# Performance work log

Measured on AMD Instinct MI355X. Metric: run time of the kernel, lower is better.

Reference implementation:

```python
import jax, jax.numpy as jnp
import numpy as np

B, T, IN, H, L, OUT, PRED, FN = 512, 96, 64, 512, 2, 1, 24, 32


def setup_inputs() -> dict:
    key = jax.random.key(0)
    ks = jax.random.split(key, 12)
    sc = 0.02
    n = lambda i, shape: jax.random.normal(ks[i], shape, jnp.float32) * sc
    return {
        "x": jax.random.normal(ks[0], (B, T, IN), jnp.float32),
        "station_id": jax.random.randint(ks[1], (B,), 0, 26, jnp.int32),
        "W_hidden": n(2, (H, IN)), "b_hidden": jnp.zeros((H,), jnp.float32),
        "embed": n(3, (26, H)),
        "W_ih": n(4, (L, 4 * H, H)), "W_hh": n(5, (L, 4 * H, H)),
        "b_ih": jnp.zeros((L, 4 * H), jnp.float32), "b_hh": jnp.zeros((L, 4 * H), jnp.float32),
        "conv_W": n(6, (FN, T - 1)), "conv_b": jnp.zeros((FN,), jnp.float32),
        "W1": n(7, (FN, H)), "b1": jnp.zeros((FN,), jnp.float32),
        "W2": n(8, (H, H + FN)), "b2": jnp.zeros((H,), jnp.float32),
        "W_out": n(9, (T * OUT, H)), "b_out": jnp.zeros((T * OUT,), jnp.float32),
    }


def _lstm(xc, W_ih, W_hh, b_ih, b_hh):
    # xc: [B, T, H]; multi-layer LSTM, PyTorch gate order i,f,g,o
    n_layers = W_ih.shape[0]
    h0 = jnp.zeros((n_layers, xc.shape[0], W_hh.shape[-1]), xc.dtype)

    def step(carry, xt):
        h, c = carry  # [L, B, H]
        inp = xt
        hs, cs = [], []
        for l in range(n_layers):
            g = inp @ W_ih[l].T + h[l] @ W_hh[l].T + b_ih[l] + b_hh[l]
            i, f, gg, o = jnp.split(g, 4, axis=-1)
            cn = jax.nn.sigmoid(f) * c[l] + jax.nn.sigmoid(i) * jnp.tanh(gg)
            hn = jax.nn.sigmoid(o) * jnp.tanh(cn)
            hs.append(hn); cs.append(cn)
            inp = hn
        return (jnp.stack(hs), jnp.stack(cs)), inp  # emit last-layer h

    _, outs = jax.lax.scan(step, (h0, h0), jnp.swapaxes(xc, 0, 1))
    return jnp.swapaxes(outs, 0, 1)  # [B, T, H] last-layer hidden states


def reference(x, station_id, W_hidden, b_hidden, embed, W_ih, W_hh, b_ih, b_hh,
              conv_W, conv_b, W1, b1, W2, b2, W_out, b_out):
    b, t, _ = x.shape
    hdim = W_hidden.shape[0]
    fn = conv_W.shape[0]
    xc = jax.nn.relu(x @ W_hidden.T + b_hidden)
    xc = xc + embed[station_id][:, None, :]
    hs_seq = _lstm(xc, W_ih, W_hh, b_ih, b_hh)          # [B, T, H]
    Hmat = jax.nn.relu(hs_seq[:, :-1, :])                # [B, T-1, H]
    htt = hs_seq[:, -1, :]                               # [B, H]
    # Conv2d(1, FN, (T-1, 1)) over [B,1,T-1,H] == contraction over time
    conv = jax.nn.relu(jnp.einsum('bth,ft->bfh', Hmat, conv_W) + conv_b[None, :, None])
    # original does .view(-1, feat_size, filter_num): raw reshape, not transpose
    feat = conv.reshape(b, hdim, fn)                     # [B, H, FN]
    w = (htt @ W1.T + b1)[:, None, :]                    # [B, 1, FN]
    alpha = jax.nn.sigmoid(jnp.sum(feat * w, axis=2))    # [B, H]
    v = jnp.sum(alpha[:, :, None] * feat, axis=1)        # [B, FN]
    new_ht = jnp.concatenate([htt, v], axis=1) @ W2.T + b2
    ypred = (new_ht @ W_out.T + b_out)[:, -PRED * OUT:]
    return ypred
```

## Files before the change

kernel.cpp:

```cpp
#include <hip/hip_runtime.h>
#include <math.h>

namespace {

constexpr int B = 512, T = 96, IN = 64, H = 512, G4 = 2048;
constexpr int FN = 32, KC = 544, NPRED = 24, TM1 = T - 1;
constexpr int BH = B * H;

typedef __attribute__((ext_vector_type(8))) short s8v;
typedef __attribute__((ext_vector_type(16))) float f16v;

__device__ __forceinline__ float sigf(float x) { return 1.0f / (1.0f + __expf(-x)); }
__device__ __forceinline__ float tanhfast(float x) {
  x = fminf(fmaxf(x, -15.f), 15.f);
  float e = __expf(2.0f * x);
  return (e - 1.0f) / (e + 1.0f);
}
__device__ __forceinline__ unsigned short bf16_rne(float f) {
  unsigned u = __float_as_uint(f);
  u += 0x7fffu + ((u >> 16) & 1u);
  return (unsigned short)(u >> 16);
}
__device__ __forceinline__ void split8(const float4& x, const float4& y, s8v& hi, s8v& lo) {
  float vs[8] = {x.x, x.y, x.z, x.w, y.x, y.y, y.z, y.w};
#pragma unroll
  for (int j = 0; j < 8; ++j) {
    unsigned ub = __float_as_uint(vs[j]);
    hi[j] = (short)(ub >> 16);
    lo[j] = (short)bf16_rne(vs[j] - __uint_as_float(ub & 0xffff0000u));
  }
}

__global__ __launch_bounds__(256) void k_xc(
    const float* __restrict__ x, const int* __restrict__ sid,
    const float* __restrict__ Wh, const float* __restrict__ bh,
    const float* __restrict__ emb, float* __restrict__ planes) {
  constexpr int RWS = 64;
  int gid = blockIdx.x;
  int half = gid & 1;
  int row0 = (gid >> 1) * RWS;
  int tid = threadIdx.x;
  int h = half * 256 + tid;
  __shared__ float sx[RWS][IN];
  {
    const float4* xsrc = (const float4*)(x + (size_t)row0 * IN);
    float4* sdst = (float4*)(&sx[0][0]);
    for (int i = tid; i < RWS * IN / 4; i += 256) sdst[i] = xsrc[i];
  }
  float4 w[16];
  const float* wr = Wh + (size_t)h * IN;
#pragma unroll
  for (int j = 0; j < 16; ++j) w[j] = *(const float4*)(wr + j * 4);
  float b0 = bh[h];
  const float* ep = emb + h;
  __syncthreads();
#pragma unroll 2
  for (int r = 0; r < RWS; ++r) {
    float a0 = b0, a1 = 0.f, a2 = 0.f, a3 = 0.f;
#pragma unroll
    for (int j = 0; j < 16; ++j) {
      float4 xv = *(const float4*)(&sx[r][j * 4]);
      a0 = fmaf(xv.x, w[j].x, a0);
      a1 = fmaf(xv.y, w[j].y, a1);
      a2 = fmaf(xv.z, w[j].z, a2);
      a3 = fmaf(xv.w, w[j].w, a3);
    }
    float acc = (a0 + a1) + (a2 + a3);
    int row = row0 + r;
    int bb = row / T, t = row % T;
    float v = fmaxf(acc, 0.f) + ep[(size_t)sid[bb] * H];
    planes[((size_t)t * B + bb) * H + h] = v;
  }
}

__global__ __launch_bounds__(256) void k_wswz(
    const float* __restrict__ Wih, const float* __restrict__ Whh,
    short* __restrict__ WFhi, short* __restrict__ WFlo) {
  int g = blockIdx.x * 256 + threadIdx.x;
  int lane = g & 63;
  int fi = g >> 6;
  int nt = fi & 3, kt = (fi >> 2) & 63, ng = (fi >> 8) & 15, layer = fi >> 12;
  int row = nt * H + ng * 32 + (lane & 31);
  int kk = kt * 16 + (lane >> 5) * 8;
  const float* src = (kk < H) ? (Wih + ((size_t)layer * G4 + row) * H + kk)
                              : (Whh + ((size_t)layer * G4 + row) * H + (kk - H));
  float4 f0 = *(const float4*)src, f1 = *(const float4*)(src + 4);
  s8v hi, lo;
  split8(f0, f1, hi, lo);
  size_t o = (size_t)fi * 512 + lane * 8;
  *(s8v*)(WFhi + o) = hi;
  *(s8v*)(WFlo + o) = lo;
}

__global__ __launch_bounds__(256, 1) void k_step(
    int tt, float* __restrict__ planes, const short* __restrict__ WFhi,
    const short* __restrict__ WFlo, short* __restrict__ hFhi,
    short* __restrict__ hFlo, const float* __restrict__ bih,
    const float* __restrict__ bhh, float* __restrict__ c0,
    float* __restrict__ c1) {
  int gid = blockIdx.x;
  int xcd = gid & 7;
  int u = gid >> 3;
  int combo = xcd * 4 + (u & 3);
  int layer = combo >> 4;
  if (layer ? (tt == 0) : (tt == T)) return;
  int ng = combo & 15;
  int b0 = (u >> 2) * 64;
  int step = layer ? (tt - 1) : tt;
  int tid = threadIdx.x, lane = tid & 63, wk = tid >> 6;
  int l31 = lane & 31, lh = lane >> 5;

  __shared__ float comb[4][4][32][32];

  const float* bi = bih + (size_t)layer * G4;
  const float* bh2 = bhh + (size_t)layer * G4;
  float* cbuf = layer ? c1 : c0;

  int rpar = (step - 1) & 1;
  const float* xbase = nullptr;
  const short *abhi = nullptr, *ablo = nullptr;
  if (layer == 0 && wk < 2) {
    xbase = planes + (size_t)step * BH + (size_t)(b0 + l31) * H + wk * 256 + lh * 8;
  } else {
    int src = (layer == 0) ? 0 : ((wk < 2) ? 0 : 1);
    int par = (layer == 0) ? rpar : ((wk < 2) ? (step & 1) : rpar);
    int kk0 = wk * 16 - ((layer == 0 || wk >= 2) ? 32 : 0);
    size_t o = ((((size_t)src * 2 + par) * 32 + kk0) * H + (b0 + l31)) * 16 + lh * 8;
    abhi = hFhi + o;
    ablo = hFlo + o;
  }

  float bias[4];
#pragma unroll
  for (int nt = 0; nt < 4; ++nt) {
    int r = nt * H + ng * 32 + l31;
    bias[nt] = bi[r] + bh2[r];
  }

  const size_t wstep = 4 * 512;
  const size_t wbase0 = ((size_t)(layer * 16 + ng) * 64 + wk * 16) * wstep + (size_t)lane * 8;
  const size_t astep = (size_t)H * 16;

  f16v acc[2][4];
#pragma unroll
  for (int rt = 0; rt < 2; ++rt)
#pragma unroll
    for (int nt = 0; nt < 4; ++nt)
#pragma unroll
      for (int e = 0; e < 16; ++e) acc[rt][nt][e] = 0.f;

  s8v a0h0, a0l0, a0h1, a0l1, b0h0, b0h1, b0h2, b0h3, b0l0, b0l1, b0l2, b0l3;
  s8v a1h0, a1l0, a1h1, a1l1, b1h0, b1h1, b1h2, b1h3, b1l0, b1l1, b1l2, b1l3;
  s8v a2h0, a2l0, a2h1, a2l1, b2h0, b2h1, b2h2, b2h3, b2l0, b2l1, b2l2, b2l3;

#define LOADW_(kq, bh0, bh1, bh2, bh3, bl0, bl1, bl2, bl3)          \
  {                                                                 \
    size_t wo = wbase0 + (size_t)(kq) * wstep;                      \
    bh0 = *(const s8v*)(WFhi + wo);                                 \
    bh1 = *(const s8v*)(WFhi + wo + 512);                           \
    bh2 = *(const s8v*)(WFhi + wo + 1024);                          \
    bh3 = *(const s8v*)(WFhi + wo + 1536);                          \
    bl0 = *(const s8v*)(WFlo + wo);                                 \
    bl1 = *(const s8v*)(WFlo + wo + 512);                           \
    bl2 = *(const s8v*)(WFlo + wo + 1024);                          \
    bl3 = *(const s8v*)(WFlo + wo + 1536);                          \
  }
#define LOADA_(kq, ah0, al0, ah1, al1)                              \
  {                                                                 \
    if (xbase) {                                                    \
      const float* ap = xbase + (kq) * 16;                          \
      float4 f0 = *(const float4*)ap, f1 = *(const float4*)(ap + 4);\
      split8(f0, f1, ah0, al0);                                     \
      const float* aq = ap + 32 * H;                                \
      float4 g0 = *(const float4*)aq, g1 = *(const float4*)(aq + 4);\
      split8(g0, g1, ah1, al1);                                     \
    } else {                                                        \
      const short* ph = abhi + (size_t)(kq) * astep;                \
      const short* pl = ablo + (size_t)(kq) * astep;                \
      ah0 = *(const s8v*)(ph);                                      \
      al0 = *(const s8v*)(pl);                                      \
      ah1 = *(const s8v*)(ph + 512);                                \
      al1 = *(const s8v*)(pl + 512);                                \
    }                                                               \
  }
#define MFMA3R_(rt, ah, al, bh0, bh1, bh2, bh3, bl0, bl1, bl2, bl3)                        \
  {                                                                                        \
    acc[rt][0] = __builtin_amdgcn_mfma_f32_32x32x16_bf16(ah, bh0, acc[rt][0], 0, 0, 0);    \
    acc[rt][1] = __builtin_amdgcn_mfma_f32_32x32x16_bf16(ah, bh1, acc[rt][1], 0, 0, 0);    \
    acc[rt][2] = __builtin_amdgcn_mfma_f32_32x32x16_bf16(ah, bh2, acc[rt][2], 0, 0, 0);    \
    acc[rt][3] = __builtin_amdgcn_mfma_f32_32x32x16_bf16(ah, bh3, acc[rt][3], 0, 0, 0);    \
    acc[rt][0] = __builtin_amdgcn_mfma_f32_32x32x16_bf16(ah, bl0, acc[rt][0], 0, 0, 0);    \
    acc[rt][1] = __builtin_amdgcn_mfma_f32_32x32x16_bf16(ah, bl1, acc[rt][1], 0, 0, 0);    \
    acc[rt][2] = __builtin_amdgcn_mfma_f32_32x32x16_bf16(ah, bl2, acc[rt][2], 0, 0, 0);    \
    acc[rt][3] = __builtin_amdgcn_mfma_f32_32x32x16_bf16(ah, bl3, acc[rt][3], 0, 0, 0);    \
    acc[rt][0] = __builtin_amdgcn_mfma_f32_32x32x16_bf16(al, bh0, acc[rt][0], 0, 0, 0);    \
    acc[rt][1] = __builtin_amdgcn_mfma_f32_32x32x16_bf16(al, bh1, acc[rt][1], 0, 0, 0);    \
    acc[rt][2] = __builtin_amdgcn_mfma_f32_32x32x16_bf16(al, bh2, acc[rt][2], 0, 0, 0);    \
    acc[rt][3] = __builtin_amdgcn_mfma_f32_32x32x16_bf16(al, bh3, acc[rt][3], 0, 0, 0);    \
  }
#define MFMA6_(ah0, al0, ah1, al1, bh0, bh1, bh2, bh3, bl0, bl1, bl2, bl3)  \
  {                                                                         \
    MFMA3R_(0, ah0, al0, bh0, bh1, bh2, bh3, bl0, bl1, bl2, bl3);           \
    MFMA3R_(1, ah1, al1, bh0, bh1, bh2, bh3, bl0, bl1, bl2, bl3);           \
  }

  LOADA_(0, a0h0, a0l0, a0h1, a0l1);
  LOADW_(0, b0h0, b0h1, b0h2, b0h3, b0l0, b0l1, b0l2, b0l3);
  LOADA_(1, a1h0, a1l0, a1h1, a1l1);
  LOADW_(1, b1h0, b1h1, b1h2, b1h3, b1l0, b1l1, b1l2, b1l3);
  LOADA_(2, a2h0, a2l0, a2h1, a2l1);
  LOADW_(2, b2h0, b2h1, b2h2, b2h3, b2l0, b2l1, b2l2, b2l3);
#pragma unroll 1
  for (int kp = 0; kp < 5; ++kp) {
    int kq = kp * 3;
    MFMA6_(a0h0, a0l0, a0h1, a0l1, b0h0, b0h1, b0h2, b0h3, b0l0, b0l1, b0l2, b0l3);
    LOADA_(kq + 3, a0h0, a0l0, a0h1, a0l1);
    LOADW_(kq + 3, b0h0, b0h1, b0h2, b0h3, b0l0, b0l1, b0l2, b0l3);
    MFMA6_(a1h0, a1l0, a1h1, a1l1, b1h0, b1h1, b1h2, b1h3, b1l0, b1l1, b1l2, b1l3);
    if (kp < 4) {
      LOADA_(kq + 4, a1h0, a1l0, a1h1, a1l1);
      LOADW_(kq + 4, b1h0, b1h1, b1h2, b1h3, b1l0, b1l1, b1l2, b1l3);
    }
    MFMA6_(a2h0, a2l0, a2h1, a2l1, b2h0, b2h1, b2h2, b2h3, b2l0, b2l1, b2l2, b2l3);
    if (kp < 4) {
      LOADA_(kq + 5, a2h0, a2l0, a2h1, a2l1);
      LOADW_(kq + 5, b2h0, b2h1, b2h2, b2h3, b2l0, b2l1, b2l2, b2l3);
    }
  }
  MFMA6_(a0h0, a0l0, a0h1, a0l1, b0h0, b0h1, b0h2, b0h3, b0l0, b0l1, b0l2, b0l3);
#undef LOADW_
#undef LOADA_
#undef MFMA3R_
#undef MFMA6_

#pragma unroll
  for (int rt = 0; rt < 2; ++rt) {
    if (rt) __syncthreads();
#pragma unroll
    for (int nt = 0; nt < 4; ++nt)
#pragma unroll
      for (int r = 0; r < 16; ++r) {
        int row = (r & 3) + 8 * (r >> 2) + 4 * lh;
        comb[nt][wk][row][l31] = acc[rt][nt][r];
      }
    __syncthreads();
    int b0p = b0 + rt * 32;
#pragma unroll
    for (int rr = 0; rr < 4; ++rr) {
      int r = wk * 4 + rr;
      int row = (r & 3) + 8 * (r >> 2) + 4 * lh;
      float g[4];
#pragma unroll
      for (int nt = 0; nt < 4; ++nt) {
        float p0 = comb[nt][0][row][l31];
        float p1 = comb[nt][1][row][l31];
        float p2 = comb[nt][2][row][l31];
        float p3 = comb[nt][3][row][l31];
        g[nt] = (p0 + p1) + (p2 + p3) + bias[nt];
      }
      size_t coff = (size_t)(b0p + row) * H + ng * 32 + l31;
      float cp = cbuf[coff];
      float cn = sigf(g[1]) * cp + sigf(g[0]) * tanhfast(g[2]);
      float hn = sigf(g[3]) * tanhfast(cn);
      cbuf[coff] = cn;
      int brow = b0p + row;
      int hcol = ng * 32 + l31;
      size_t o = ((((size_t)layer * 2 + (step & 1)) * 32 + (hcol >> 4)) * H + brow) * 16 + (hcol & 15);
      unsigned ub = __float_as_uint(hn);
      hFhi[o] = (short)(ub >> 16);
      hFlo[o] = (short)bf16_rne(hn - __uint_as_float(ub & 0xffff0000u));
      if (layer) planes[(size_t)step * BH + (size_t)brow * H + hcol] = hn;
    }
  }
}

__global__ __launch_bounds__(256) void k_conv(
    const float* __restrict__ hs, const float* __restrict__ cW,
    const float* __restrict__ cb, float* __restrict__ feat) {
  int b = blockIdx.x >> 2;
  int h0 = (blockIdx.x & 3) * 128;
  int tid = threadIdx.x;
  __shared__ float sW[TM1][FN];
  for (int i = tid; i < TM1 * FN; i += 256) sW[i >> 5][i & 31] = cW[(i & 31) * TM1 + (i >> 5)];
  __syncthreads();
  int hl = tid & 127, fg = (tid >> 7) * 16;
  float acc[16];
#pragma unroll
  for (int j = 0; j < 16; ++j) acc[j] = cb[fg + j];
  const float* hp = hs + (size_t)b * H + h0 + hl;
  for (int t = 0; t < TM1; ++t) {
    float v = fmaxf(hp[(size_t)t * BH], 0.f);
#pragma unroll
    for (int j = 0; j < 16; ++j) acc[j] = fmaf(v, sW[t][fg + j], acc[j]);
  }
#pragma unroll
  for (int j = 0; j < 16; ++j)
    feat[(size_t)b * (FN * H) + (size_t)(fg + j) * H + h0 + hl] = fmaxf(acc[j], 0.f);
}

__global__ __launch_bounds__(256) void k_attn(
    const float* __restrict__ hs, const float* __restrict__ feat,
    const float* __restrict__ W1, const float* __restrict__ b1,
    const float* __restrict__ W2, const float* __restrict__ b2,
    const float* __restrict__ Wout, const float* __restrict__ bout,
    float* __restrict__ out) {
  int b = blockIdx.x, tid = threadIdx.x;
  __shared__ float sh[H], sa[H], snew[H], sw[FN], sv[FN], red[256];
  const float* htt = hs + (size_t)(T - 1) * BH + (size_t)b * H;
  for (int i = tid; i < H; i += 256) sh[i] = htt[i];
  __syncthreads();
  {
    int f = tid >> 3, sl = tid & 7;
    const float* w1 = W1 + (size_t)f * H;
    float p = 0.f;
    for (int k = sl * 64; k < sl * 64 + 64; ++k) p = fmaf(sh[k], w1[k], p);
    p += __shfl_xor(p, 1); p += __shfl_xor(p, 2); p += __shfl_xor(p, 4);
    if (sl == 0) sw[f] = p + b1[f];
  }
  __syncthreads();
  const float* fb = feat + (size_t)b * (FN * H);
  for (int i = tid; i < H; i += 256) {
    const float* fr = fb + (size_t)i * FN;
    float p = 0.f;
#pragma unroll
    for (int j = 0; j < FN; j += 4) {
      float4 fv = *(const float4*)(fr + j);
      p = fmaf(fv.x, sw[j], p);
      p = fmaf(fv.y, sw[j + 1], p);
      p = fmaf(fv.z, sw[j + 2], p);
      p = fmaf(fv.w, sw[j + 3], p);
    }
    sa[i] = sigf(p);
  }
  __syncthreads();
  {
    int j = tid & 31, isl = tid >> 5;
    float p = 0.f;
    for (int i = isl * 64; i < isl * 64 + 64; ++i) p = fmaf(sa[i], fb[(size_t)i * FN + j], p);
    red[tid] = p;
  }
  __syncthreads();
  if (tid < 128) red[tid] += red[tid + 128];
  __syncthreads();
  if (tid < 64) red[tid] += red[tid + 64];
  __syncthreads();
  if (tid < 32) sv[tid] = red[tid] + red[tid + 32];
  __syncthreads();
  for (int h = tid; h < H; h += 256) {
    const float* w2 = W2 + (size_t)h * KC;
    float p = b2[h];
#pragma unroll 4
    for (int k = 0; k < H; k += 4) {
      float4 wv = *(const float4*)(w2 + k);
      float4 shv = *(const float4*)(sh + k);
      p = fmaf(shv.x, wv.x, p);
      p = fmaf(shv.y, wv.y, p);
      p = fmaf(shv.z, wv.z, p);
      p = fmaf(shv.w, wv.w, p);
    }
#pragma unroll
    for (int j = 0; j < FN; j += 4) {
      float4 wv = *(const float4*)(w2 + H + j);
      p = fmaf(sv[j], wv.x, p);
      p = fmaf(sv[j + 1], wv.y, p);
      p = fmaf(sv[j + 2], wv.z, p);
      p = fmaf(sv[j + 3], wv.w, p);
    }
    snew[h] = p;
  }
  __syncthreads();
  if (tid < NPRED * 8) {
    int p = tid >> 3, sl = tid & 7;
    const float* wo = Wout + (size_t)(T - NPRED + p) * H;
    float sacc = 0.f;
    for (int k = sl * 64; k < sl * 64 + 64; ++k) sacc = fmaf(snew[k], wo[k], sacc);
    sacc += __shfl_xor(sacc, 1); sacc += __shfl_xor(sacc, 2); sacc += __shfl_xor(sacc, 4);
    if (sl == 0) out[(size_t)b * NPRED + p] = sacc + bout[T - NPRED + p];
  }
}

}

extern "C" void kernel_launch(void* const* d_in, const int* in_sizes, int n_in,
                              void* d_out, int out_size, void* d_ws, size_t ws_size,
                              hipStream_t stream) {
  const float* x    = (const float*)d_in[0];
  const int*   sid  = (const int*)d_in[1];
  const float* Wh   = (const float*)d_in[2];
  const float* bh   = (const float*)d_in[3];
  const float* emb  = (const float*)d_in[4];
  const float* Wih  = (const float*)d_in[5];
  const float* Whh  = (const float*)d_in[6];
  const float* bih  = (const float*)d_in[7];
  const float* bhh  = (const float*)d_in[8];
  const float* cW   = (const float*)d_in[9];
  const float* cb   = (const float*)d_in[10];
  const float* W1   = (const float*)d_in[11];
  const float* b1   = (const float*)d_in[12];
  const float* W2   = (const float*)d_in[13];
  const float* b2   = (const float*)d_in[14];
  const float* Wout = (const float*)d_in[15];
  const float* bout = (const float*)d_in[16];
  float* out = (float*)d_out;

  constexpr size_t HFE = (size_t)2 * 2 * 32 * H * 16;
  float* planes = (float*)d_ws;
  short* WFhi = (short*)(planes + (size_t)T * BH);
  short* WFlo = WFhi + (size_t)8192 * 512;
  short* hFhi = WFlo + (size_t)8192 * 512;
  short* hFlo = hFhi + HFE;
  float* cst = (float*)(hFlo + HFE);
  float* c0 = cst;
  float* c1 = cst + BH;
  float* feat = c1 + BH;
  size_t need = (size_t)T * BH * 4 + (size_t)8192 * 512 * 2 * 2 + HFE * 2 * 2 +
                2 * (size_t)BH * 4 + (size_t)B * FN * H * 4;
  if (ws_size < need) return;

  hipMemsetAsync(hFhi, 0, HFE * 2 * 2 + 2 * (size_t)BH * 4, stream);
  k_xc<<<(B * T / 64) * 2, 256, 0, stream>>>(x, sid, Wh, bh, emb, planes);
  k_wswz<<<2048, 256, 0, stream>>>(Wih, Whh, WFhi, WFlo);

  for (int tt = 0; tt <= T; ++tt)
    k_step<<<256, 256, 0, stream>>>(tt, planes, WFhi, WFlo, hFhi, hFlo, bih, bhh, c0, c1);

  k_conv<<<B * 4, 256, 0, stream>>>(planes, cW, cb, feat);
  k_attn<<<B, 256, 0, stream>>>(planes, feat, W1, b1, W2, b2, Wout, bout, out);
}
```

Measured before the change: 2.324 ms.

## Repartition LSTM step kernel: smaller batch tiles, per-wave gate tiles, split-K by two

```diff
diff --git a/kernel.cpp b/kernel.cpp
--- a/kernel.cpp
+++ b/kernel.cpp
@@ -92,7 +92,7 @@
   *(s8v*)(WFlo + o) = lo;
 }
 
-__global__ __launch_bounds__(256, 1) void k_step(
+__global__ __launch_bounds__(512, 4) void k_step5(
     int tt, float* __restrict__ planes, const short* __restrict__ WFhi,
     const short* __restrict__ WFlo, short* __restrict__ hFhi,
     short* __restrict__ hFlo, const float* __restrict__ bih,
@@ -105,172 +105,122 @@
   int layer = combo >> 4;
   if (layer ? (tt == 0) : (tt == T)) return;
   int ng = combo & 15;
-  int b0 = (u >> 2) * 64;
+  int bt2 = u >> 2;
+  int b0 = bt2 * 32;
   int step = layer ? (tt - 1) : tt;
-  int tid = threadIdx.x, lane = tid & 63, wk = tid >> 6;
+  int tid = threadIdx.x, lane = tid & 63;
+  int wv = tid >> 6;
+  int nt = wv & 3, kqh = wv >> 2;
   int l31 = lane & 31, lh = lane >> 5;
 
-  __shared__ float comb[4][4][32][32];
+  __shared__ float comb[2][4][32][32];
 
   const float* bi = bih + (size_t)layer * G4;
   const float* bh2 = bhh + (size_t)layer * G4;
   float* cbuf = layer ? c1 : c0;
 
   int rpar = (step - 1) & 1;
+  bool use_x = (layer == 0) && (kqh == 0);
   const float* xbase = nullptr;
   const short *abhi = nullptr, *ablo = nullptr;
-  if (layer == 0 && wk < 2) {
-    xbase = planes + (size_t)step * BH + (size_t)(b0 + l31) * H + wk * 256 + lh * 8;
+  if (use_x) {
+    xbase = planes + (size_t)step * BH + (size_t)(b0 + l31) * H + lh * 8;
   } else {
-    int src = (layer == 0) ? 0 : ((wk < 2) ? 0 : 1);
-    int par = (layer == 0) ? rpar : ((wk < 2) ? (step & 1) : rpar);
-    int kk0 = wk * 16 - ((layer == 0 || wk >= 2) ? 32 : 0);
-    size_t o = ((((size_t)src * 2 + par) * 32 + kk0) * H + (b0 + l31)) * 16 + lh * 8;
+    int src = (layer == 0) ? 0 : ((kqh == 0) ? 0 : 1);
+    int par = (layer == 0) ? rpar : ((kqh == 0) ? (step & 1) : rpar);
+    size_t o = ((((size_t)src * 2 + par) * 32) * H + (size_t)(b0 + l31)) * 16 + lh * 8;
     abhi = hFhi + o;
     ablo = hFlo + o;
   }
 
   float bias[4];
 #pragma unroll
-  for (int nt = 0; nt < 4; ++nt) {
-    int r = nt * H + ng * 32 + l31;
-    bias[nt] = bi[r] + bh2[r];
+  for (int q = 0; q < 4; ++q) {
+    int r = q * H + ng * 32 + l31;
+    bias[q] = bi[r] + bh2[r];
   }
 
   const size_t wstep = 4 * 512;
-  const size_t wbase0 = ((size_t)(layer * 16 + ng) * 64 + wk * 16) * wstep + (size_t)lane * 8;
+  const size_t wb = (((size_t)(layer * 16 + ng) * 64 + (size_t)kqh * 32) * 4 + nt) * 512 +
+                    (size_t)lane * 8;
   const size_t astep = (size_t)H * 16;
 
-  f16v acc[2][4];
-#pragma unroll
-  for (int rt = 0; rt < 2; ++rt)
-#pragma unroll
-    for (int nt = 0; nt < 4; ++nt)
-#pragma unroll
-      for (int e = 0; e < 16; ++e) acc[rt][nt][e] = 0.f;
-
-  s8v a0h0, a0l0, a0h1, a0l1, b0h0, b0h1, b0h2, b0h3, b0l0, b0l1, b0l2, b0l3;
-  s8v a1h0, a1l0, a1h1, a1l1, b1h0, b1h1, b1h2, b1h3, b1l0, b1l1, b1l2, b1l3;
-  s8v a2h0, a2l0, a2h1, a2l1, b2h0, b2h1, b2h2, b2h3, b2l0, b2l1, b2l2, b2l3;
-
-#define LOADW_(kq, bh0, bh1, bh2, bh3, bl0, bl1, bl2, bl3)          \
-  {                                                                 \
-    size_t wo = wbase0 + (size_t)(kq) * wstep;                      \
-    bh0 = *(const s8v*)(WFhi + wo);                                 \
-    bh1 = *(const s8v*)(WFhi + wo + 512);                           \
-    bh2 = *(const s8v*)(WFhi + wo + 1024);                          \
-    bh3 = *(const s8v*)(WFhi + wo + 1536);                          \
-    bl0 = *(const s8v*)(WFlo + wo);                                 \
-    bl1 = *(const s8v*)(WFlo + wo + 512);                           \
-    bl2 = *(const s8v*)(WFlo + wo + 1024);                          \
-    bl3 = *(const s8v*)(WFlo + wo + 1536);                          \
-  }
-#define LOADA_(kq, ah0, al0, ah1, al1)                              \
-  {                                                                 \
-    if (xbase) {                                                    \
-      const float* ap = xbase + (kq) * 16;                          \
-      float4 f0 = *(const float4*)ap, f1 = *(const float4*)(ap + 4);\
-      split8(f0, f1, ah0, al0);                                     \
-      const float* aq = ap + 32 * H;                                \
-      float4 g0 = *(const float4*)aq, g1 = *(const float4*)(aq + 4);\
-      split8(g0, g1, ah1, al1);                                     \
-    } else {                                                        \
-      const short* ph = abhi + (size_t)(kq) * astep;                \
-      const short* pl = ablo + (size_t)(kq) * astep;                \
-      ah0 = *(const s8v*)(ph);                                      \
-      al0 = *(const s8v*)(pl);                                      \
-      ah1 = *(const s8v*)(ph + 512);                                \
-      al1 = *(const s8v*)(pl + 512);                                \
-    }                                                               \
-  }
-#define MFMA3R_(rt, ah, al, bh0, bh1, bh2, bh3, bl0, bl1, bl2, bl3)                        \
-  {                                                                                        \
-    acc[rt][0] = __builtin_amdgcn_mfma_f32_32x32x16_bf16(ah, bh0, acc[rt][0], 0, 0, 0);    \
-    acc[rt][1] = __builtin_amdgcn_mfma_f32_32x32x16_bf16(ah, bh1, acc[rt][1], 0, 0, 0);    \
-    acc[rt][2] = __builtin_amdgcn_mfma_f32_32x32x16_bf16(ah, bh2, acc[rt][2], 0, 0, 0);    \
-    acc[rt][3] = __builtin_amdgcn_mfma_f32_32x32x16_bf16(ah, bh3, acc[rt][3], 0, 0, 0);    \
-    acc[rt][0] = __builtin_amdgcn_mfma_f32_32x32x16_bf16(ah, bl0, acc[rt][0], 0, 0, 0);    \
-    acc[rt][1] = __builtin_amdgcn_mfma_f32_32x32x16_bf16(ah, bl1, acc[rt][1], 0, 0, 0);    \
-    acc[rt][2] = __builtin_amdgcn_mfma_f32_32x32x16_bf16(ah, bl2, acc[rt][2], 0, 0, 0);    \
-    acc[rt][3] = __builtin_amdgcn_mfma_f32_32x32x16_bf16(ah, bl3, acc[rt][3], 0, 0, 0);    \
-    acc[rt][0] = __builtin_amdgcn_mfma_f32_32x32x16_bf16(al, bh0, acc[rt][0], 0, 0, 0);    \
-    acc[rt][1] = __builtin_amdgcn_mfma_f32_32x32x16_bf16(al, bh1, acc[rt][1], 0, 0, 0);    \
-    acc[rt][2] = __builtin_amdgcn_mfma_f32_32x32x16_bf16(al, bh2, acc[rt][2], 0, 0, 0);    \
-    acc[rt][3] = __builtin_amdgcn_mfma_f32_32x32x16_bf16(al, bh3, acc[rt][3], 0, 0, 0);    \
-  }
-#define MFMA6_(ah0, al0, ah1, al1, bh0, bh1, bh2, bh3, bl0, bl1, bl2, bl3)  \
-  {                                                                         \
-    MFMA3R_(0, ah0, al0, bh0, bh1, bh2, bh3, bl0, bl1, bl2, bl3);           \
-    MFMA3R_(1, ah1, al1, bh0, bh1, bh2, bh3, bl0, bl1, bl2, bl3);           \
-  }
-
-  LOADA_(0, a0h0, a0l0, a0h1, a0l1);
-  LOADW_(0, b0h0, b0h1, b0h2, b0h3, b0l0, b0l1, b0l2, b0l3);
-  LOADA_(1, a1h0, a1l0, a1h1, a1l1);
-  LOADW_(1, b1h0, b1h1, b1h2, b1h3, b1l0, b1l1, b1l2, b1l3);
-  LOADA_(2, a2h0, a2l0, a2h1, a2l1);
-  LOADW_(2, b2h0, b2h1, b2h2, b2h3, b2l0, b2l1, b2l2, b2l3);
+  f16v acc;
+#pragma unroll
+  for (int e = 0; e < 16; ++e) acc[e] = 0.f;
+
+  s8v w0h, w0l, a0h, a0l;
+  s8v w1h, w1l, a1h, a1l;
+  s8v w2h, w2l, a2h, a2l;
+
+#define LOADS_(i, wh_, wl_, ah_, al_)                                 \
+  {                                                                   \
+    size_t wo = wb + (size_t)(i) * wstep;                             \
+    wh_ = *(const s8v*)(WFhi + wo);                                   \
+    wl_ = *(const s8v*)(WFlo + wo);                                   \
+    if (use_x) {                                                      \
+      const float* ap = xbase + (i) * 16;                             \
+      float4 f0 = *(const float4*)ap, f1 = *(const float4*)(ap + 4);  \
+      split8(f0, f1, ah_, al_);                                       \
+    } else {                                                          \
+      ah_ = *(const s8v*)(abhi + (size_t)(i) * astep);                \
+      al_ = *(const s8v*)(ablo + (size_t)(i) * astep);                \
+    }                                                                 \
+  }
+#define MM3_(wh_, wl_, ah_, al_)                                          \
+  {                                                                       \
+    acc = __builtin_amdgcn_mfma_f32_32x32x16_bf16(ah_, wh_, acc, 0, 0, 0);\
+    acc = __builtin_amdgcn_mfma_f32_32x32x16_bf16(ah_, wl_, acc, 0, 0, 0);\
+    acc = __builtin_amdgcn_mfma_f32_32x32x16_bf16(al_, wh_, acc, 0, 0, 0);\
+  }
+
+  LOADS_(0, w0h, w0l, a0h, a0l);
+  LOADS_(1, w1h, w1l, a1h, a1l);
+  LOADS_(2, w2h, w2l, a2h, a2l);
 #pragma unroll 1
-  for (int kp = 0; kp < 5; ++kp) {
-    int kq = kp * 3;
-    MFMA6_(a0h0, a0l0, a0h1, a0l1, b0h0, b0h1, b0h2, b0h3, b0l0, b0l1, b0l2, b0l3);
-    LOADA_(kq + 3, a0h0, a0l0, a0h1, a0l1);
-    LOADW_(kq + 3, b0h0, b0h1, b0h2, b0h3, b0l0, b0l1, b0l2, b0l3);
-    MFMA6_(a1h0, a1l0, a1h1, a1l1, b1h0, b1h1, b1h2, b1h3, b1l0, b1l1, b1l2, b1l3);
-    if (kp < 4) {
-      LOADA_(kq + 4, a1h0, a1l0, a1h1, a1l1);
-      LOADW_(kq + 4, b1h0, b1h1, b1h2, b1h3, b1l0, b1l1, b1l2, b1l3);
-    }
-    MFMA6_(a2h0, a2l0, a2h1, a2l1, b2h0, b2h1, b2h2, b2h3, b2l0, b2l1, b2l2, b2l3);
-    if (kp < 4) {
-      LOADA_(kq + 5, a2h0, a2l0, a2h1, a2l1);
-      LOADW_(kq + 5, b2h0, b2h1, b2h2, b2h3, b2l0, b2l1, b2l2, b2l3);
-    }
-  }
-  MFMA6_(a0h0, a0l0, a0h1, a0l1, b0h0, b0h1, b0h2, b0h3, b0l0, b0l1, b0l2, b0l3);
-#undef LOADW_
-#undef LOADA_
-#undef MFMA3R_
-#undef MFMA6_
-
-#pragma unroll
-  for (int rt = 0; rt < 2; ++rt) {
-    if (rt) __syncthreads();
-#pragma unroll
-    for (int nt = 0; nt < 4; ++nt)
-#pragma unroll
-      for (int r = 0; r < 16; ++r) {
-        int row = (r & 3) + 8 * (r >> 2) + 4 * lh;
-        comb[nt][wk][row][l31] = acc[rt][nt][r];
-      }
-    __syncthreads();
-    int b0p = b0 + rt * 32;
-#pragma unroll
-    for (int rr = 0; rr < 4; ++rr) {
-      int r = wk * 4 + rr;
-      int row = (r & 3) + 8 * (r >> 2) + 4 * lh;
-      float g[4];
-#pragma unroll
-      for (int nt = 0; nt < 4; ++nt) {
-        float p0 = comb[nt][0][row][l31];
-        float p1 = comb[nt][1][row][l31];
-        float p2 = comb[nt][2][row][l31];
-        float p3 = comb[nt][3][row][l31];
-        g[nt] = (p0 + p1) + (p2 + p3) + bias[nt];
-      }
-      size_t coff = (size_t)(b0p + row) * H + ng * 32 + l31;
-      float cp = cbuf[coff];
-      float cn = sigf(g[1]) * cp + sigf(g[0]) * tanhfast(g[2]);
-      float hn = sigf(g[3]) * tanhfast(cn);
-      cbuf[coff] = cn;
-      int brow = b0p + row;
-      int hcol = ng * 32 + l31;
-      size_t o = ((((size_t)layer * 2 + (step & 1)) * 32 + (hcol >> 4)) * H + brow) * 16 + (hcol & 15);
-      unsigned ub = __float_as_uint(hn);
-      hFhi[o] = (short)(ub >> 16);
-      hFlo[o] = (short)bf16_rne(hn - __uint_as_float(ub & 0xffff0000u));
-      if (layer) planes[(size_t)step * BH + (size_t)brow * H + hcol] = hn;
-    }
+  for (int kp = 0; kp < 10; ++kp) {
+    int i = kp * 3;
+    MM3_(w0h, w0l, a0h, a0l);
+    LOADS_(i + 3, w0h, w0l, a0h, a0l);
+    MM3_(w1h, w1l, a1h, a1l);
+    LOADS_(i + 4, w1h, w1l, a1h, a1l);
+    MM3_(w2h, w2l, a2h, a2l);
+    if (kp < 9) LOADS_(i + 5, w2h, w2l, a2h, a2l);
+  }
+  MM3_(w0h, w0l, a0h, a0l);
+  MM3_(w1h, w1l, a1h, a1l);
+#undef LOADS_
+#undef MM3_
+
+#pragma unroll
+  for (int r = 0; r < 16; ++r) {
+    int row = (r & 3) + 8 * (r >> 2) + 4 * lh;
+    comb[kqh][nt][row][l31] = acc[r];
+  }
+  __syncthreads();
+
+  int col = tid & 31;
+  int r0 = tid >> 5;
+#pragma unroll
+  for (int j = 0; j < 2; ++j) {
+    int row = r0 + j * 16;
+    float g[4];
+#pragma unroll
+    for (int q = 0; q < 4; ++q)
+      g[q] = (comb[0][q][row][col] + comb[1][q][row][col]) + bias[q];
+    int brow = b0 + row;
+    int hcol = ng * 32 + col;
+    size_t coff = (size_t)brow * H + hcol;
+    float cp = cbuf[coff];
+    float cn = sigf(g[1]) * cp + sigf(g[0]) * tanhfast(g[2]);
+    float hn = sigf(g[3]) * tanhfast(cn);
+    cbuf[coff] = cn;
+    size_t o = ((((size_t)layer * 2 + (step & 1)) * 32 + (hcol >> 4)) * H + brow) * 16 +
+               (hcol & 15);
+    unsigned ub = __float_as_uint(hn);
+    hFhi[o] = (short)(ub >> 16);
+    hFlo[o] = (short)bf16_rne(hn - __uint_as_float(ub & 0xffff0000u));
+    if (layer) planes[(size_t)step * BH + (size_t)brow * H + hcol] = hn;
   }
 }
 
@@ -422,7 +372,7 @@
   k_wswz<<<2048, 256, 0, stream>>>(Wih, Whh, WFhi, WFlo);
 
   for (int tt = 0; tt <= T; ++tt)
-    k_step<<<256, 256, 0, stream>>>(tt, planes, WFhi, WFlo, hFhi, hFlo, bih, bhh, c0, c1);
+    k_step5<<<512, 512, 0, stream>>>(tt, planes, WFhi, WFlo, hFhi, hFlo, bih, bhh, c0, c1);
 
   k_conv<<<B * 4, 256, 0, stream>>>(planes, cW, cb, feat);
   k_attn<<<B, 256, 0, stream>>>(planes, feat, W1, b1, W2, b2, Wout, bout, out);
```

Measured after the change: 3.163 ms. 1.36x slower.
